# Optimization experiments

Hardware: AMD Instinct MI355X
Metric: run time of the kernel (lower is better)

## Reference

```python
import jax, jax.numpy as jnp
import numpy as np

N = 50000      # nodes
E = 800000     # directed edges (avg degree 16)
F_IN = 128     # in_channels
HID = 256      # hidden_channels
OUT = 40       # out_channels (classes)


def setup_inputs() -> dict:
    key = jax.random.key(0)
    ks = jax.random.split(key, 6)
    x = jax.random.normal(ks[0], (N, F_IN), dtype=jnp.float32)
    edge_index = jax.random.randint(ks[1], (2, E), 0, N, dtype=jnp.int32)
    W1 = jax.random.normal(ks[2], (F_IN, HID), dtype=jnp.float32) * (1.0 / np.sqrt(F_IN))
    b1 = jnp.zeros((HID,), jnp.float32)
    W2 = jax.random.normal(ks[3], (HID, HID), dtype=jnp.float32) * (1.0 / np.sqrt(HID))
    b2 = jnp.zeros((HID,), jnp.float32)
    Wc = jax.random.normal(ks[4], (HID, OUT), dtype=jnp.float32) * (1.0 / np.sqrt(HID))
    bc = jnp.zeros((OUT,), jnp.float32)
    return {"x": x, "W1": W1, "b1": b1, "W2": W2, "b2": b2,
            "Wc": Wc, "bc": bc, "edge_index": edge_index}


def _gcn_conv(x, W, b, src, dst, norm):
    # PyG GCNConv: linear transform, then normalized sparse aggregation, then bias.
    h = x @ W                                    # [N, H]
    msg = h[src] * norm[:, None]                 # [E+N, H] gather + scale
    agg = jax.ops.segment_sum(msg, dst, num_segments=N)  # scatter-add
    return agg + b


def reference(x, W1, b1, W2, b2, Wc, bc, edge_index):
    # add self-loops (GCNConv default add_self_loops=True)
    loops = jnp.arange(N, dtype=edge_index.dtype)
    src = jnp.concatenate([edge_index[0], loops])
    dst = jnp.concatenate([edge_index[1], loops])
    # symmetric normalization D^-1/2 A D^-1/2 (degree counted at dst)
    deg = jax.ops.segment_sum(jnp.ones_like(dst, dtype=jnp.float32), dst,
                              num_segments=N)
    dinv = jax.lax.rsqrt(jnp.maximum(deg, 1.0))  # deg >= 1 due to self-loops
    norm = dinv[src] * dinv[dst]                 # [E+N]
    # layer 1 + ReLU (dropout is identity in eval mode)
    h = jax.nn.relu(_gcn_conv(x, W1, b1, src, dst, norm))
    # layer 2 + ReLU
    h = jax.nn.relu(_gcn_conv(h, W2, b2, src, dst, norm))
    # dense classifier
    return h @ Wc + bc  # [N, OUT]
```

## Files before the change

kernel.cpp:

```cpp
#include <hip/hip_runtime.h>

#define NNODES 50000
#define NEDGES 800000
#define F_IN   128
#define HID    256
#define NOUT   40
#define NOUT_PAD 48
#define NBLK_SCAN ((NNODES + 255) / 256)
#define NBLK_CAST 6250
#define NBLK_DEG  3125

typedef __attribute__((ext_vector_type(8))) _Float16 f16x8;
typedef __attribute__((ext_vector_type(4))) float f32x4;
typedef __attribute__((ext_vector_type(4))) unsigned short u16x4;
typedef __attribute__((ext_vector_type(8))) unsigned short u16x8;

__device__ __forceinline__ unsigned short f2h(float f) {
  return __builtin_bit_cast(unsigned short, (_Float16)f);
}
__device__ __forceinline__ float h2f(unsigned short u) {
  return (float)__builtin_bit_cast(_Float16, u);
}


__global__ __launch_bounds__(256) void k_pre(const float* __restrict__ X,
                                             unsigned short* __restrict__ Xh,
                                             const int* __restrict__ dst,
                                             int* __restrict__ count) {
  if (blockIdx.x < NBLK_CAST) {
    int i = blockIdx.x * 256 + threadIdx.x;
    float4 v = *reinterpret_cast<const float4*>(X + (size_t)i * 4);
    ushort4 o;
    o.x = f2h(v.x); o.y = f2h(v.y); o.z = f2h(v.z); o.w = f2h(v.w);
    *reinterpret_cast<ushort4*>(Xh + (size_t)i * 4) = o;
  } else {
    int e = (blockIdx.x - NBLK_CAST) * 256 + threadIdx.x;
    if (e < NEDGES) atomicAdd(&count[dst[e]], 1);
  }
}


__global__ __launch_bounds__(256) void k_scan1(const int* __restrict__ count,
                                               int* __restrict__ rowstart,
                                               int* __restrict__ bsum,
                                               float* __restrict__ dinv) {
  __shared__ int tmp[256];
  int t = threadIdx.x;
  int i = blockIdx.x * 256 + t;
  int v = (i < NNODES) ? count[i] : 0;
  if (i < NNODES) dinv[i] = rsqrtf((float)(v + 1));
  tmp[t] = v;
  __syncthreads();
  for (int off = 1; off < 256; off <<= 1) {
    int x = (t >= off) ? tmp[t - off] : 0;
    __syncthreads();
    tmp[t] += x;
    __syncthreads();
  }
  if (i < NNODES) rowstart[i] = tmp[t] - v;
  if (t == 255) bsum[blockIdx.x] = tmp[255];
}

__global__ __launch_bounds__(256) void k_scan2(const int* __restrict__ bsum,
                                               int* __restrict__ boff) {
  __shared__ int tmp[256];
  int t = threadIdx.x;
  int v = (t < NBLK_SCAN) ? bsum[t] : 0;
  tmp[t] = v;
  __syncthreads();
  for (int off = 1; off < 256; off <<= 1) {
    int x = (t >= off) ? tmp[t - off] : 0;
    __syncthreads();
    tmp[t] += x;
    __syncthreads();
  }
  if (t < NBLK_SCAN) boff[t] = tmp[t] - v;
}

__global__ __launch_bounds__(256) void k_scan3(int* __restrict__ rowstart,
                                               const int* __restrict__ boff) {
  int i = blockIdx.x * 256 + threadIdx.x;
  if (i < NNODES) rowstart[i] += boff[blockIdx.x];
  if (i == 0) rowstart[NNODES] = NEDGES;
}

__global__ __launch_bounds__(256) void k_scatter(const int* __restrict__ src,
                                                 const int* __restrict__ dst,
                                                 const int* __restrict__ rowstart,
                                                 int* __restrict__ cursor,
                                                 int* __restrict__ csr) {
  int e = blockIdx.x * 256 + threadIdx.x;
  if (e >= NEDGES) return;
  int d = dst[e];
  int p = rowstart[d] + atomicAdd(&cursor[d], 1);
  csr[p] = src[e];
}


__global__ __launch_bounds__(256) void k_prep3(const float* __restrict__ W1,
                                               const float* __restrict__ W2,
                                               const float* __restrict__ Wc,
                                               unsigned short* __restrict__ T1,
                                               unsigned short* __restrict__ T2,
                                               unsigned short* __restrict__ Tc) {
  int b = blockIdx.x;
  if (b < 128) {
    int idx = b * 256 + threadIdx.x;
    int n = idx >> 7, k = idx & 127;
    T1[idx] = f2h(W1[(size_t)k * HID + n]);
  } else if (b < 384) {
    int idx = (b - 128) * 256 + threadIdx.x;
    int n = idx >> 8, k = idx & 255;
    T2[idx] = f2h(W2[(size_t)k * HID + n]);
  } else {
    int idx = (b - 384) * 256 + threadIdx.x;
    int n = idx >> 8, k = idx & 255;
    float v = (n < NOUT) ? Wc[(size_t)k * NOUT + n] : 0.f;
    Tc[idx] = f2h(v);
  }
}


__global__ __launch_bounds__(256) void k_agg1(const unsigned short* __restrict__ X,
                                              const int* __restrict__ rowstart,
                                              const int* __restrict__ csr,
                                              const float* __restrict__ dinv,
                                              uint2* __restrict__ Y) {
  int wave = threadIdx.x >> 6, lane = threadIdx.x & 63;
  int node = blockIdx.x * 4 + wave;
  if (node >= NNODES) return;
  int half = lane >> 5, l32 = lane & 31;
  float di = dinv[node];
  float a[4] = {0.f, 0.f, 0.f, 0.f};
  int e = rowstart[node], end = rowstart[node + 1];
  for (; e + 8 <= end; e += 8) {
    int s0 = csr[e + 0 + half], s1 = csr[e + 2 + half];
    int s2 = csr[e + 4 + half], s3 = csr[e + 6 + half];
    float w0 = dinv[s0] * di, w1 = dinv[s1] * di;
    float w2 = dinv[s2] * di, w3 = dinv[s3] * di;
    u16x4 r0 = *reinterpret_cast<const u16x4*>(X + (size_t)s0 * F_IN + l32 * 4);
    u16x4 r1 = *reinterpret_cast<const u16x4*>(X + (size_t)s1 * F_IN + l32 * 4);
    u16x4 r2 = *reinterpret_cast<const u16x4*>(X + (size_t)s2 * F_IN + l32 * 4);
    u16x4 r3 = *reinterpret_cast<const u16x4*>(X + (size_t)s3 * F_IN + l32 * 4);
#pragma unroll
    for (int k = 0; k < 4; k++) {
      a[k] = fmaf(h2f(r0[k]), w0, a[k]);
      a[k] = fmaf(h2f(r1[k]), w1, a[k]);
      a[k] = fmaf(h2f(r2[k]), w2, a[k]);
      a[k] = fmaf(h2f(r3[k]), w3, a[k]);
    }
  }
  for (; e + 2 <= end; e += 2) {
    int s = csr[e + half];
    float w = dinv[s] * di;
    u16x4 r = *reinterpret_cast<const u16x4*>(X + (size_t)s * F_IN + l32 * 4);
#pragma unroll
    for (int k = 0; k < 4; k++) a[k] = fmaf(h2f(r[k]), w, a[k]);
  }
  if (e < end) {
    int s = csr[e];
    float w = half ? 0.f : dinv[s] * di;
    u16x4 r = *reinterpret_cast<const u16x4*>(X + (size_t)s * F_IN + l32 * 4);
#pragma unroll
    for (int k = 0; k < 4; k++) a[k] = fmaf(h2f(r[k]), w, a[k]);
  }
#pragma unroll
  for (int k = 0; k < 4; k++) a[k] += __shfl_xor(a[k], 32);
  if (half == 0) {
    u16x4 self = *reinterpret_cast<const u16x4*>(X + (size_t)node * F_IN + l32 * 4);
    float dd = di * di;
#pragma unroll
    for (int k = 0; k < 4; k++) a[k] = fmaf(h2f(self[k]), dd, a[k]);
    uint2 o;
    o.x = (unsigned)f2h(a[0]) | ((unsigned)f2h(a[1]) << 16);
    o.y = (unsigned)f2h(a[2]) | ((unsigned)f2h(a[3]) << 16);
    Y[(size_t)node * 32 + l32] = o;
  }
}


__global__ __launch_bounds__(256) void k_agg2(const unsigned short* __restrict__ H,
                                              const int* __restrict__ rowstart,
                                              const int* __restrict__ csr,
                                              const float* __restrict__ dinv,
                                              uint4* __restrict__ Y) {
  int wave = threadIdx.x >> 6, lane = threadIdx.x & 63;
  int node = blockIdx.x * 4 + wave;
  if (node >= NNODES) return;
  int half = lane >> 5, l32 = lane & 31;
  float di = dinv[node];
  float a[8] = {0.f, 0.f, 0.f, 0.f, 0.f, 0.f, 0.f, 0.f};
  int e = rowstart[node], end = rowstart[node + 1];
  for (; e + 8 <= end; e += 8) {
    int s0 = csr[e + 0 + half], s1 = csr[e + 2 + half];
    int s2 = csr[e + 4 + half], s3 = csr[e + 6 + half];
    float w0 = dinv[s0] * di, w1 = dinv[s1] * di;
    float w2 = dinv[s2] * di, w3 = dinv[s3] * di;
    u16x8 r0 = *reinterpret_cast<const u16x8*>(H + (size_t)s0 * HID + l32 * 8);
    u16x8 r1 = *reinterpret_cast<const u16x8*>(H + (size_t)s1 * HID + l32 * 8);
    u16x8 r2 = *reinterpret_cast<const u16x8*>(H + (size_t)s2 * HID + l32 * 8);
    u16x8 r3 = *reinterpret_cast<const u16x8*>(H + (size_t)s3 * HID + l32 * 8);
#pragma unroll
    for (int k = 0; k < 8; k++) {
      a[k] = fmaf(h2f(r0[k]), w0, a[k]);
      a[k] = fmaf(h2f(r1[k]), w1, a[k]);
      a[k] = fmaf(h2f(r2[k]), w2, a[k]);
      a[k] = fmaf(h2f(r3[k]), w3, a[k]);
    }
  }
  for (; e + 2 <= end; e += 2) {
    int s = csr[e + half];
    float w = dinv[s] * di;
    u16x8 r = *reinterpret_cast<const u16x8*>(H + (size_t)s * HID + l32 * 8);
#pragma unroll
    for (int k = 0; k < 8; k++) a[k] = fmaf(h2f(r[k]), w, a[k]);
  }
  if (e < end) {
    int s = csr[e];
    float w = half ? 0.f : dinv[s] * di;
    u16x8 r = *reinterpret_cast<const u16x8*>(H + (size_t)s * HID + l32 * 8);
#pragma unroll
    for (int k = 0; k < 8; k++) a[k] = fmaf(h2f(r[k]), w, a[k]);
  }
#pragma unroll
  for (int k = 0; k < 8; k++) a[k] += __shfl_xor(a[k], 32);
  if (half == 0) {
    u16x8 self = *reinterpret_cast<const u16x8*>(H + (size_t)node * HID + l32 * 8);
    float dd = di * di;
#pragma unroll
    for (int k = 0; k < 8; k++) a[k] = fmaf(h2f(self[k]), dd, a[k]);
    uint4 o;
    o.x = (unsigned)f2h(a[0]) | ((unsigned)f2h(a[1]) << 16);
    o.y = (unsigned)f2h(a[2]) | ((unsigned)f2h(a[3]) << 16);
    o.z = (unsigned)f2h(a[4]) | ((unsigned)f2h(a[5]) << 16);
    o.w = (unsigned)f2h(a[6]) | ((unsigned)f2h(a[7]) << 16);
    Y[(size_t)node * 32 + l32] = o;
  }
}


template <int RELU, int OMODE>
__global__ __launch_bounds__(256) void k_mgemm(const unsigned short* __restrict__ Ag,
                                               const unsigned short* __restrict__ Btg,
                                               const float* __restrict__ bias,
                                               void* __restrict__ Cout,
                                               int M, int Nc, int K) {
  __shared__ unsigned short Ah[2][128 * 40];
  __shared__ unsigned short Bh[2][128 * 40];
  int tid = threadIdx.x;
  int lane = tid & 63, w = tid >> 6;
  int wr = w >> 1, wc = w & 1;
  int bm = blockIdx.x * 128, bn = blockIdx.y * 128;
  int l15 = lane & 15, kg = lane >> 4;
  int row0 = tid >> 2, kq0 = (tid & 3) * 8;
  int gm0 = bm + row0, gm1 = bm + row0 + 64;

  f32x4 zero = {0.f, 0.f, 0.f, 0.f};
  f32x4 acc[4][4];
#pragma unroll
  for (int i = 0; i < 4; i++)
#pragma unroll
    for (int j = 0; j < 4; j++) acc[i][j] = zero;

  uint4 ra0, ra1, rb0, rb1;
  const uint4 z4 = {0, 0, 0, 0};
#define LOADT(KT)                                                                    \
  {                                                                                  \
    ra0 = z4; ra1 = z4;                                                              \
    if (gm0 < M) ra0 = *reinterpret_cast<const uint4*>(Ag + (size_t)gm0 * K + (KT) + kq0); \
    if (gm1 < M) ra1 = *reinterpret_cast<const uint4*>(Ag + (size_t)gm1 * K + (KT) + kq0); \
    rb0 = *reinterpret_cast<const uint4*>(Btg + (size_t)(bn + row0) * K + (KT) + kq0);     \
    rb1 = *reinterpret_cast<const uint4*>(Btg + (size_t)(bn + row0 + 64) * K + (KT) + kq0);\
  }
#define STORET(B)                                                       \
  {                                                                     \
    *reinterpret_cast<uint4*>(&Ah[B][row0 * 40 + kq0]) = ra0;           \
    *reinterpret_cast<uint4*>(&Ah[B][(row0 + 64) * 40 + kq0]) = ra1;    \
    *reinterpret_cast<uint4*>(&Bh[B][row0 * 40 + kq0]) = rb0;           \
    *reinterpret_cast<uint4*>(&Bh[B][(row0 + 64) * 40 + kq0]) = rb1;    \
  }

  LOADT(0);
  STORET(0);
  __syncthreads();
  int nt = K >> 5, cur = 0;
  for (int t = 0; t < nt; t++) {
    bool pf = (t + 1 < nt);
    if (pf) LOADT((t + 1) << 5);
    f16x8 fa[4], fb[4];
#pragma unroll
    for (int f = 0; f < 4; f++) {
      fa[f] = *reinterpret_cast<const f16x8*>(&Ah[cur][(wr * 64 + f * 16 + l15) * 40 + kg * 8]);
      fb[f] = *reinterpret_cast<const f16x8*>(&Bh[cur][(wc * 64 + f * 16 + l15) * 40 + kg * 8]);
    }
#pragma unroll
    for (int i = 0; i < 4; i++)
#pragma unroll
      for (int j = 0; j < 4; j++)
        acc[i][j] = __builtin_amdgcn_mfma_f32_16x16x32_f16(fa[i], fb[j], acc[i][j], 0, 0, 0);
    if (pf) STORET(cur ^ 1);
    __syncthreads();
    cur ^= 1;
  }
#undef LOADT
#undef STORET

  int r0 = kg * 4;
#pragma unroll
  for (int i = 0; i < 4; i++) {
    int gmBase = bm + wr * 64 + i * 16 + r0;
#pragma unroll
    for (int r = 0; r < 4; r++) {
      int gm = gmBase + r;
      if (gm >= M) continue;
#pragma unroll
      for (int j = 0; j < 4; j++) {
        int gn = bn + wc * 64 + j * 16 + l15;
        if (gn >= Nc) continue;
        float v = acc[i][j][r] + bias[gn];
        if (RELU) v = fmaxf(v, 0.f);
        size_t o = (size_t)gm * Nc + gn;
        if (OMODE == 0) ((float*)Cout)[o] = v;
        else            ((unsigned short*)Cout)[o] = f2h(v);
      }
    }
  }
}


__global__ __launch_bounds__(256) void k_cls(const unsigned short* __restrict__ Ag,
                                             const unsigned short* __restrict__ Btg,
                                             const float* __restrict__ bias,
                                             float* __restrict__ C, int M) {
  __shared__ unsigned short As[256 * 40];
  __shared__ unsigned short Bs[48 * 40];
  int tid = threadIdx.x;
  int lane = tid & 63, w = tid >> 6;
  int l15 = lane & 15, kg = lane >> 4;
  int bm = blockIdx.x * 256;

  f32x4 zero = {0.f, 0.f, 0.f, 0.f};
  f32x4 acc[4][3];
#pragma unroll
  for (int i = 0; i < 4; i++)
#pragma unroll
    for (int j = 0; j < 3; j++) acc[i][j] = zero;

  for (int kt = 0; kt < HID; kt += 32) {
#pragma unroll
    for (int it = 0; it < 4; it++) {
      int c = tid + it * 256;
      int row = c >> 2, kq = (c & 3) * 8;
      int gm = bm + row;
      uint4 v = {0, 0, 0, 0};
      if (gm < M) v = *reinterpret_cast<const uint4*>(Ag + (size_t)gm * HID + kt + kq);
      *reinterpret_cast<uint4*>(&As[row * 40 + kq]) = v;
    }
    if (tid < 192) {
      int row = tid >> 2, kq = (tid & 3) * 8;
      *reinterpret_cast<uint4*>(&Bs[row * 40 + kq]) =
          *reinterpret_cast<const uint4*>(Btg + (size_t)row * HID + kt + kq);
    }
    __syncthreads();
    f16x8 fa[4], fb[3];
#pragma unroll
    for (int f = 0; f < 4; f++)
      fa[f] = *reinterpret_cast<const f16x8*>(&As[(w * 64 + f * 16 + l15) * 40 + kg * 8]);
#pragma unroll
    for (int j = 0; j < 3; j++)
      fb[j] = *reinterpret_cast<const f16x8*>(&Bs[(j * 16 + l15) * 40 + kg * 8]);
#pragma unroll
    for (int i = 0; i < 4; i++)
#pragma unroll
      for (int j = 0; j < 3; j++)
        acc[i][j] = __builtin_amdgcn_mfma_f32_16x16x32_f16(fa[i], fb[j], acc[i][j], 0, 0, 0);
    __syncthreads();
  }

  int r0 = kg * 4;
#pragma unroll
  for (int i = 0; i < 4; i++) {
    int gmBase = bm + w * 64 + i * 16 + r0;
#pragma unroll
    for (int r = 0; r < 4; r++) {
      int gm = gmBase + r;
      if (gm >= M) continue;
#pragma unroll
      for (int j = 0; j < 3; j++) {
        int gn = j * 16 + l15;
        if (gn >= NOUT) continue;
        C[(size_t)gm * NOUT + gn] = acc[i][j][r] + bias[gn];
      }
    }
  }
}


extern "C" void kernel_launch(void* const* d_in, const int* in_sizes, int n_in,
                              void* d_out, int out_size, void* d_ws, size_t ws_size,
                              hipStream_t stream) {
  (void)in_sizes; (void)n_in; (void)out_size; (void)ws_size;
  const float* x  = (const float*)d_in[0];
  const float* W1 = (const float*)d_in[1];
  const float* b1 = (const float*)d_in[2];
  const float* W2 = (const float*)d_in[3];
  const float* b2 = (const float*)d_in[4];
  const float* Wc = (const float*)d_in[5];
  const float* bc = (const float*)d_in[6];
  const int* edge = (const int*)d_in[7];
  const int* srcE = edge;
  const int* dstE = edge + NEDGES;
  float* out = (float*)d_out;

  char* ws = (char*)d_ws;
  int*   count    = (int*)(ws + 0);
  int*   cursor   = (int*)(ws + 200064);
  int*   rowstart = (int*)(ws + 400128);
  float* dinv     = (float*)(ws + 600320);
  int*   csr      = (int*)(ws + 800384);
  int*   bsum     = (int*)(ws + 4000512);
  int*   boff     = (int*)(ws + 4001536);
  unsigned short* W1t = (unsigned short*)(ws + 4002560);
  unsigned short* W2t = (unsigned short*)(ws + 4068096);
  unsigned short* Wct = (unsigned short*)(ws + 4199168);
  unsigned short* xh  = (unsigned short*)(ws + 4264704);
  unsigned short* aggx = (unsigned short*)(ws + 17064704);
  unsigned short* h1   = (unsigned short*)(ws + 29864704);
  unsigned short* aggh = (unsigned short*)(ws + 55464704);
  unsigned short* h2   = (unsigned short*)(ws + 81064704);

  hipMemsetAsync(ws, 0, 400128, stream);

  k_pre<<<NBLK_CAST + NBLK_DEG, 256, 0, stream>>>(x, xh, dstE, count);
  k_scan1<<<NBLK_SCAN, 256, 0, stream>>>(count, rowstart, bsum, dinv);
  k_scan2<<<1, 256, 0, stream>>>(bsum, boff);
  k_scan3<<<NBLK_SCAN, 256, 0, stream>>>(rowstart, boff);
  k_scatter<<<(NEDGES + 255) / 256, 256, 0, stream>>>(srcE, dstE, rowstart, cursor, csr);
  k_prep3<<<432, 256, 0, stream>>>(W1, W2, Wc, W1t, W2t, Wct);

  k_agg1<<<(NNODES + 3) / 4, 256, 0, stream>>>(xh, rowstart, csr, dinv, (uint2*)aggx);
  {
    dim3 grid((NNODES + 127) / 128, HID / 128);
    k_mgemm<1, 1><<<grid, 256, 0, stream>>>(aggx, W1t, b1, (void*)h1, NNODES, HID, F_IN);
  }
  k_agg2<<<(NNODES + 3) / 4, 256, 0, stream>>>(h1, rowstart, csr, dinv, (uint4*)aggh);
  {
    dim3 grid((NNODES + 127) / 128, HID / 128);
    k_mgemm<1, 1><<<grid, 256, 0, stream>>>(aggh, W2t, b2, (void*)h2, NNODES, HID, HID);
  }
  k_cls<<<(NNODES + 255) / 256, 256, 0, stream>>>(h2, Wct, bc, out, NNODES);
}
```

Baseline: 351.7 us.

## Partition degree/scatter atomics by node range per XCD and fuse prep kernels

Degree counting and CSR scatter now have each block scan an edge chunk and handle only destinations in one of eight node ranges selected by block index modulo eight, so atomics for a given node range come from one group of blocks. Weight transposition is folded into the pre-pass kernel, and the separate offset-fixup scan pass is removed by adding block offsets when rows are read in the scatter and aggregation kernels. The aim is to cut atomic contention across caches and launch overhead, at the cost of reading the destination array eight times.

```diff
diff --git a/kernel.cpp b/kernel.cpp
--- a/kernel.cpp
+++ b/kernel.cpp
@@ -5,10 +5,12 @@
 #define F_IN   128
 #define HID    256
 #define NOUT   40
-#define NOUT_PAD 48
 #define NBLK_SCAN ((NNODES + 255) / 256)
 #define NBLK_CAST 6250
-#define NBLK_DEG  3125
+#define NBLK_DEG  2048
+#define NBLK_PREP 432
+#define EDGE_CHUNK 3125
+#define NODES_PER_G 6250
 
 typedef __attribute__((ext_vector_type(8))) _Float16 f16x8;
 typedef __attribute__((ext_vector_type(4))) float f32x4;
@@ -26,16 +28,46 @@
 __global__ __launch_bounds__(256) void k_pre(const float* __restrict__ X,
                                              unsigned short* __restrict__ Xh,
                                              const int* __restrict__ dst,
-                                             int* __restrict__ count) {
-  if (blockIdx.x < NBLK_CAST) {
-    int i = blockIdx.x * 256 + threadIdx.x;
+                                             int* __restrict__ count,
+                                             const float* __restrict__ W1,
+                                             const float* __restrict__ W2,
+                                             const float* __restrict__ Wc,
+                                             unsigned short* __restrict__ T1,
+                                             unsigned short* __restrict__ T2,
+                                             unsigned short* __restrict__ Tc) {
+  int b = blockIdx.x, t = threadIdx.x;
+  if (b < NBLK_CAST) {
+    int i = b * 256 + t;
     float4 v = *reinterpret_cast<const float4*>(X + (size_t)i * 4);
     ushort4 o;
     o.x = f2h(v.x); o.y = f2h(v.y); o.z = f2h(v.z); o.w = f2h(v.w);
     *reinterpret_cast<ushort4*>(Xh + (size_t)i * 4) = o;
+  } else if (b < NBLK_CAST + NBLK_DEG) {
+    int db = b - NBLK_CAST;
+    int g = b & 7;
+    int chunk = db >> 3;
+    int lo = g * NODES_PER_G, hi = lo + NODES_PER_G;
+    int base = chunk * EDGE_CHUNK;
+    for (int i = base + t; i < base + EDGE_CHUNK; i += 256) {
+      int d = dst[i];
+      if (d >= lo && d < hi) atomicAdd(&count[d], 1);
+    }
   } else {
-    int e = (blockIdx.x - NBLK_CAST) * 256 + threadIdx.x;
-    if (e < NEDGES) atomicAdd(&count[dst[e]], 1);
+    int pb = b - NBLK_CAST - NBLK_DEG;
+    if (pb < 128) {
+      int idx = pb * 256 + t;
+      int n = idx >> 7, k = idx & 127;
+      T1[idx] = f2h(W1[(size_t)k * HID + n]);
+    } else if (pb < 384) {
+      int idx = (pb - 128) * 256 + t;
+      int n = idx >> 8, k = idx & 255;
+      T2[idx] = f2h(W2[(size_t)k * HID + n]);
+    } else {
+      int idx = (pb - 384) * 256 + t;
+      int n = idx >> 8, k = idx & 255;
+      float v = (n < NOUT) ? Wc[(size_t)k * NOUT + n] : 0.f;
+      Tc[idx] = f2h(v);
+    }
   }
 }
 
@@ -77,52 +109,30 @@
   if (t < NBLK_SCAN) boff[t] = tmp[t] - v;
 }
 
-__global__ __launch_bounds__(256) void k_scan3(int* __restrict__ rowstart,
-                                               const int* __restrict__ boff) {
-  int i = blockIdx.x * 256 + threadIdx.x;
-  if (i < NNODES) rowstart[i] += boff[blockIdx.x];
-  if (i == 0) rowstart[NNODES] = NEDGES;
-}
 
 __global__ __launch_bounds__(256) void k_scatter(const int* __restrict__ src,
                                                  const int* __restrict__ dst,
                                                  const int* __restrict__ rowstart,
+                                                 const int* __restrict__ boff,
                                                  int* __restrict__ cursor,
                                                  int* __restrict__ csr) {
-  int e = blockIdx.x * 256 + threadIdx.x;
-  if (e >= NEDGES) return;
-  int d = dst[e];
-  int p = rowstart[d] + atomicAdd(&cursor[d], 1);
-  csr[p] = src[e];
-}
-
-
-__global__ __launch_bounds__(256) void k_prep3(const float* __restrict__ W1,
-                                               const float* __restrict__ W2,
-                                               const float* __restrict__ Wc,
-                                               unsigned short* __restrict__ T1,
-                                               unsigned short* __restrict__ T2,
-                                               unsigned short* __restrict__ Tc) {
-  int b = blockIdx.x;
-  if (b < 128) {
-    int idx = b * 256 + threadIdx.x;
-    int n = idx >> 7, k = idx & 127;
-    T1[idx] = f2h(W1[(size_t)k * HID + n]);
-  } else if (b < 384) {
-    int idx = (b - 128) * 256 + threadIdx.x;
-    int n = idx >> 8, k = idx & 255;
-    T2[idx] = f2h(W2[(size_t)k * HID + n]);
-  } else {
-    int idx = (b - 384) * 256 + threadIdx.x;
-    int n = idx >> 8, k = idx & 255;
-    float v = (n < NOUT) ? Wc[(size_t)k * NOUT + n] : 0.f;
-    Tc[idx] = f2h(v);
+  int g = blockIdx.x & 7;
+  int chunk = blockIdx.x >> 3;
+  int lo = g * NODES_PER_G, hi = lo + NODES_PER_G;
+  int base = chunk * EDGE_CHUNK;
+  for (int i = base + threadIdx.x; i < base + EDGE_CHUNK; i += 256) {
+    int d = dst[i];
+    if (d >= lo && d < hi) {
+      int p = rowstart[d] + boff[d >> 8] + atomicAdd(&cursor[d], 1);
+      csr[p] = src[i];
+    }
   }
 }
 
 
 __global__ __launch_bounds__(256) void k_agg1(const unsigned short* __restrict__ X,
                                               const int* __restrict__ rowstart,
+                                              const int* __restrict__ boff,
                                               const int* __restrict__ csr,
                                               const float* __restrict__ dinv,
                                               uint2* __restrict__ Y) {
@@ -132,7 +142,8 @@
   int half = lane >> 5, l32 = lane & 31;
   float di = dinv[node];
   float a[4] = {0.f, 0.f, 0.f, 0.f};
-  int e = rowstart[node], end = rowstart[node + 1];
+  int e = rowstart[node] + boff[node >> 8];
+  int end = (node + 1 < NNODES) ? rowstart[node + 1] + boff[(node + 1) >> 8] : NEDGES;
   for (; e + 8 <= end; e += 8) {
     int s0 = csr[e + 0 + half], s1 = csr[e + 2 + half];
     int s2 = csr[e + 4 + half], s3 = csr[e + 6 + half];
@@ -181,6 +192,7 @@
 
 __global__ __launch_bounds__(256) void k_agg2(const unsigned short* __restrict__ H,
                                               const int* __restrict__ rowstart,
+                                              const int* __restrict__ boff,
                                               const int* __restrict__ csr,
                                               const float* __restrict__ dinv,
                                               uint4* __restrict__ Y) {
@@ -190,7 +202,8 @@
   int half = lane >> 5, l32 = lane & 31;
   float di = dinv[node];
   float a[8] = {0.f, 0.f, 0.f, 0.f, 0.f, 0.f, 0.f, 0.f};
-  int e = rowstart[node], end = rowstart[node + 1];
+  int e = rowstart[node] + boff[node >> 8];
+  int end = (node + 1 < NNODES) ? rowstart[node + 1] + boff[(node + 1) >> 8] : NEDGES;
   for (; e + 8 <= end; e += 8) {
     int s0 = csr[e + 0 + half], s1 = csr[e + 2 + half];
     int s2 = csr[e + 4 + half], s3 = csr[e + 6 + half];
@@ -431,19 +444,18 @@
 
   hipMemsetAsync(ws, 0, 400128, stream);
 
-  k_pre<<<NBLK_CAST + NBLK_DEG, 256, 0, stream>>>(x, xh, dstE, count);
+  k_pre<<<NBLK_CAST + NBLK_DEG + NBLK_PREP, 256, 0, stream>>>(
+      x, xh, dstE, count, W1, W2, Wc, W1t, W2t, Wct);
   k_scan1<<<NBLK_SCAN, 256, 0, stream>>>(count, rowstart, bsum, dinv);
   k_scan2<<<1, 256, 0, stream>>>(bsum, boff);
-  k_scan3<<<NBLK_SCAN, 256, 0, stream>>>(rowstart, boff);
-  k_scatter<<<(NEDGES + 255) / 256, 256, 0, stream>>>(srcE, dstE, rowstart, cursor, csr);
-  k_prep3<<<432, 256, 0, stream>>>(W1, W2, Wc, W1t, W2t, Wct);
-
-  k_agg1<<<(NNODES + 3) / 4, 256, 0, stream>>>(xh, rowstart, csr, dinv, (uint2*)aggx);
+  k_scatter<<<NBLK_DEG, 256, 0, stream>>>(srcE, dstE, rowstart, boff, cursor, csr);
+
+  k_agg1<<<(NNODES + 3) / 4, 256, 0, stream>>>(xh, rowstart, boff, csr, dinv, (uint2*)aggx);
   {
     dim3 grid((NNODES + 127) / 128, HID / 128);
     k_mgemm<1, 1><<<grid, 256, 0, stream>>>(aggx, W1t, b1, (void*)h1, NNODES, HID, F_IN);
   }
-  k_agg2<<<(NNODES + 3) / 4, 256, 0, stream>>>(h1, rowstart, csr, dinv, (uint4*)aggh);
+  k_agg2<<<(NNODES + 3) / 4, 256, 0, stream>>>(h1, rowstart, boff, csr, dinv, (uint4*)aggh);
   {
     dim3 grid((NNODES + 127) / 128, HID / 128);
     k_mgemm<1, 1><<<grid, 256, 0, stream>>>(aggh, W2t, b2, (void*)h2, NNODES, HID, HID);
```

New measurement: 343.3 us. 2.4% less time.
